# Kernel optimization log

Measured on AMD Instinct MI355X. Metric: run time of the kernel, lower is better.

Reference implementation:

```python
import jax, jax.numpy as jnp
import numpy as np

# ---- hash-grid encoder constants (instant-NGP style, nr_levels=24 from source) ----
L_LEVELS = 24
F_FEAT = 2
T_SIZE = 1 << 19          # hashmap entries per level
BASE_RES = 16
MAX_RES = 2048
IN_CH = 3
N_PTS = 524288
GEOM = 32
MIN_OFFSET = 1e-4
BB = 2.0                  # bb_sides
RES = np.floor(BASE_RES * np.exp(np.arange(L_LEVELS) * np.log(MAX_RES / BASE_RES) / (L_LEVELS - 1))).astype(np.float32)


def hash_encode(points, table):
    # points: [N,3] in bb [-BB/2, BB/2]; table: [L, T, F]
    N = points.shape[0]
    x = points / BB + 0.5                         # normalize to [0,1]
    res = jnp.asarray(RES)                        # [L]
    scaled = x[None, :, :] * res[:, None, None]   # [L,N,3]
    pos0f = jnp.floor(scaled)
    frac = scaled - pos0f                         # [L,N,3]
    pos0 = pos0f.astype(jnp.uint32)
    p0 = jnp.uint32(1); p1 = jnp.uint32(2654435761); p2 = jnp.uint32(805459861)
    mask = jnp.uint32(T_SIZE - 1)
    lvl = jnp.arange(L_LEVELS)[:, None]
    out = jnp.zeros((L_LEVELS, N, F_FEAT), points.dtype)
    for corner in range(8):                       # fixed 8-corner trilinear loop
        off = np.array([(corner >> d) & 1 for d in range(3)])
        c = pos0 + jnp.asarray(off, dtype=jnp.uint32)
        idx = ((c[..., 0] * p0) ^ (c[..., 1] * p1) ^ (c[..., 2] * p2)) & mask  # [L,N]
        feats = table[lvl, idx.astype(jnp.int32)]                              # [L,N,F]
        w = jnp.prod(jnp.where(jnp.asarray(off, bool), frac, 1.0 - frac), axis=-1)  # [L,N]
        out = out + w[..., None] * feats
    return out.transpose(1, 0, 2).reshape(N, L_LEVELS * F_FEAT)  # [N, 48]


def setup_inputs() -> dict:
    key = jax.random.key(0)
    ks = jax.random.split(key, 12)
    points = jax.random.uniform(ks[0], (N_PTS, IN_CH), dtype=jnp.float32)
    hash_table = jax.random.uniform(ks[1], (L_LEVELS, T_SIZE, F_FEAT), jnp.float32, -1e-4, 1e-4)
    D_ENC = L_LEVELS * F_FEAT  # 48
    def lin(k, fi, fo):
        kw, kb = jax.random.split(k)
        return (jax.random.normal(kw, (fi, fo), jnp.float32) / np.sqrt(fi),
                jax.random.normal(kb, (fo,), jnp.float32) * 0.01)
    W0, b0 = lin(ks[2], D_ENC, 32)
    W1, b1 = lin(ks[3], 32, 32)
    W2, b2 = lin(ks[4], 32, 32)
    W3, b3 = lin(ks[5], 32, 1 + GEOM)
    # two per-offset MLPs (geom_feat -> 32 -> 1), batched as grouped weights [K=2,...]
    eps_W0 = jax.random.normal(ks[6], (2, GEOM, 32), jnp.float32) / np.sqrt(GEOM)
    eps_b0 = jax.random.normal(ks[7], (2, 32), jnp.float32) * 0.01
    eps_W1 = jax.random.normal(ks[8], (2, 32, 1), jnp.float32) / np.sqrt(32)
    eps_b1 = jax.random.normal(ks[9], (2, 1), jnp.float32) * 0.01
    return {"points": points, "hash_table": hash_table,
            "W0": W0, "b0": b0, "W1": W1, "b1": b1, "W2": W2, "b2": b2, "W3": W3, "b3": b3,
            "eps_W0": eps_W0, "eps_b0": eps_b0, "eps_W1": eps_W1, "eps_b1": eps_b1}


def reference(points, hash_table, W0, b0, W1, b1, W2, b2, W3, b3, eps_W0, eps_b0, eps_W1, eps_b1):
    enc = hash_encode(points, hash_table)                 # [N,48]
    h = jax.nn.relu(enc @ W0 + b0)
    h = jax.nn.relu(h @ W1 + b1)
    h = jax.nn.relu(h @ W2 + b2)
    pred = h @ W3 + b3                                    # [N, 1+GEOM]
    sdf = pred[:, 0:1]                                    # [N,1]
    geom_feats = pred[:, 1:]                              # [N,GEOM]
    # grouped per-offset MLPs: k indexes the 2 offset heads
    he = jax.nn.relu(jnp.einsum('nf,kfh->nkh', geom_feats, eps_W0) + eps_b0[None])
    eps = (jnp.einsum('nkh,kho->nko', he, eps_W1) + eps_b1[None]).squeeze(-1)  # [N,2]
    nr_outer = 1
    inner_eps = jax.nn.softplus(eps[:, nr_outer:])        # [N,1]
    outer_eps = -jax.nn.softplus(eps[:, :nr_outer])       # [N,1]
    cum_outer = jnp.cumsum(outer_eps, axis=1) - MIN_OFFSET
    cum_inner = jnp.flip(jnp.cumsum(inner_eps, axis=1) + MIN_OFFSET, axis=1)
    sdfs = jnp.concatenate([sdf + cum_inner, sdf, sdf + cum_outer], axis=1)[..., None]   # [N,3,1]
    offsets = jnp.concatenate([inner_eps, jnp.zeros_like(sdf), outer_eps], axis=1)[..., None]
    return sdfs, offsets, geom_feats
```

## Files before the change

### kernel.cpp

```cpp
#include <hip/hip_runtime.h>
#include <math.h>
#include <stdint.h>

#define NPTS   524288
#define TSZ    524288u
#define HMASK  (TSZ - 1u)
#define PRIME1 2654435761u
#define PRIME2 805459861u
#define NLVL   24

typedef float    v4f __attribute__((ext_vector_type(4)));
typedef _Float16 v4h __attribute__((ext_vector_type(4)));

#define MFMA16(A,B,C) __builtin_amdgcn_mfma_f32_16x16x16f16((A),(B),(C),0,0,0)

struct ResParams { float r[NLVL]; };

__device__ __forceinline__ uint32_t pack_f16x2(float a, float b) {
    union { _Float16 h[2]; uint32_t u; } c;
    c.h[0] = (_Float16)a; c.h[1] = (_Float16)b;
    return c.u;
}

__device__ __forceinline__ float softplus_f(float x) {
    return fmaxf(x, 0.f) + log1pf(expf(-fabsf(x)));
}

__global__ __launch_bounds__(256)
void hash_gather_pass(const float* __restrict__ points,
                      const float* __restrict__ table,
                      uint32_t* __restrict__ enc, ResParams rp)
{
    const int bid   = blockIdx.x;
    const int xcd   = bid & 7;
    const int j     = bid >> 3;
    const int lvl   = ((j >> 9) << 3) + xcd;
    const int chunk = j & 511;
    const float res = rp.r[lvl];
    const float* __restrict__ tl = table + (size_t)lvl * (size_t)(TSZ * 2u);
    uint32_t* __restrict__ el = enc + (size_t)lvl * (size_t)NPTS;
    const int pbase = chunk * 1024 + threadIdx.x;

    #pragma unroll
    for (int k = 0; k < 4; ++k) {
        const int p = pbase + k * 256;
        const float x0 = points[p * 3 + 0] * 0.5f + 0.5f;
        const float y0 = points[p * 3 + 1] * 0.5f + 0.5f;
        const float z0 = points[p * 3 + 2] * 0.5f + 0.5f;
        const float sx = x0 * res, sy = y0 * res, sz = z0 * res;
        const float fx = floorf(sx), fy = floorf(sy), fz = floorf(sz);
        const float tx = sx - fx,  ty = sy - fy,  tz = sz - fz;
        const uint32_t cx = (uint32_t)fx, cy = (uint32_t)fy, cz = (uint32_t)fz;
        const uint32_t hy0 = cy * PRIME1, hy1 = (cy + 1u) * PRIME1;
        const uint32_t hz0 = cz * PRIME2, hz1 = (cz + 1u) * PRIME2;
        const float wy[2] = {1.f - ty, ty};
        const float wz[2] = {1.f - tz, tz};
        const float wx0 = 1.f - tx, wx1 = tx;
        const bool cx_even = (cx & 1u) == 0u;

        float a0 = 0.f, a1 = 0.f;
        #pragma unroll
        for (int yz = 0; yz < 4; ++yz) {
            const uint32_t dy = (uint32_t)(yz & 1);
            const uint32_t dz = (uint32_t)(yz >> 1);
            const uint32_t h  = (dy ? hy1 : hy0) ^ (dz ? hz1 : hz0);
            const uint32_t i0 = (cx ^ h) & HMASK;
            const uint32_t i1 = ((cx + 1u) ^ h) & HMASK;
            float e0x, e0y, e1x, e1y;
            if (cx_even) {
                const float4 f4 = *reinterpret_cast<const float4*>(tl + (size_t)(i0 & ~1u) * 2u);
                const bool lo = (i0 & 1u) == 0u;
                e0x = lo ? f4.x : f4.z;  e0y = lo ? f4.y : f4.w;
                e1x = lo ? f4.z : f4.x;  e1y = lo ? f4.w : f4.y;
            } else {
                const float2 fa = *reinterpret_cast<const float2*>(tl + (size_t)i0 * 2u);
                const float2 fb = *reinterpret_cast<const float2*>(tl + (size_t)i1 * 2u);
                e0x = fa.x; e0y = fa.y; e1x = fb.x; e1y = fb.y;
            }
            const float wyz = wy[dy] * wz[dz];
            const float w0 = wyz * wx0, w1 = wyz * wx1;
            a0 = fmaf(w0, e0x, fmaf(w1, e1x, a0));
            a1 = fmaf(w0, e0y, fmaf(w1, e1y, a1));
        }
        el[p] = pack_f16x2(a0 * 1024.f, a1 * 1024.f);
    }
}

#define SW0T   0
#define SW1T   3328
#define SW2T   5632
#define SW3T   7936
#define SET    11392
#define SB0    18048
#define SB1    18176
#define SB2    18304
#define SB3    18432
#define SEB0   18624
#define SEW1   18880
#define SEB1   19136
#define SGEOM  19152
#define SMB    28368

__global__ __launch_bounds__(256)
void mlp_mfma(const uint32_t* __restrict__ enc,
              const float* __restrict__ W0, const float* __restrict__ b0,
              const float* __restrict__ W1, const float* __restrict__ b1,
              const float* __restrict__ W2, const float* __restrict__ b2,
              const float* __restrict__ W3, const float* __restrict__ b3,
              const float* __restrict__ eW0, const float* __restrict__ eb0,
              const float* __restrict__ eW1, const float* __restrict__ eb1,
              float* __restrict__ out)
{
    __shared__ __align__(16) unsigned char sm[SMB];
    _Float16* const w0t = (_Float16*)(sm + SW0T);
    _Float16* const w1t = (_Float16*)(sm + SW1T);
    _Float16* const w2t = (_Float16*)(sm + SW2T);
    _Float16* const w3t = (_Float16*)(sm + SW3T);
    _Float16* const et  = (_Float16*)(sm + SET);
    float* const b0s  = (float*)(sm + SB0);
    float* const b1s  = (float*)(sm + SB1);
    float* const b2s  = (float*)(sm + SB2);
    float* const b3s  = (float*)(sm + SB3);
    float* const eb0s = (float*)(sm + SEB0);
    float* const ew1s = (float*)(sm + SEW1);
    float* const eb1s = (float*)(sm + SEB1);

    const int tid = threadIdx.x;

    for (int i = tid; i < 1536; i += 256) { const int k = i >> 5, o = i & 31;
        w0t[o * 52 + k] = (_Float16)(W0[i] * (1.f / 1024.f)); }
    for (int i = tid; i < 1024; i += 256) { const int k = i >> 5, o = i & 31;
        w1t[o * 36 + k] = (_Float16)W1[i];
        w2t[o * 36 + k] = (_Float16)W2[i]; }
    for (int i = tid; i < 1536; i += 256) { const int o = i >> 5, k = i & 31;
        w3t[o * 36 + k] = (o < 33) ? (_Float16)W3[k * 33 + o] : (_Float16)0.f; }
    for (int i = tid; i < 3328; i += 256) {
        const int hd = i / 1664, rem = i - hd * 1664;
        const int hh = rem / 52, o = rem % 52;
        et[i] = (o >= 1 && o <= 32) ? (_Float16)eW0[hd * 1024 + (o - 1) * 32 + hh]
                                    : (_Float16)0.f;
    }
    for (int i = tid; i < 32; i += 256) { b0s[i] = b0[i]; b1s[i] = b1[i]; b2s[i] = b2[i]; }
    for (int i = tid; i < 48; i += 256) { b3s[i] = (i < 33) ? b3[i] : 0.f; }
    for (int i = tid; i < 64; i += 256) { eb0s[i] = eb0[i]; ew1s[i] = eW1[i]; }
    if (tid < 2) eb1s[tid] = eb1[tid];
    __syncthreads();

    const int wv = tid >> 6, l = tid & 63, g = l >> 4, lm = l & 15;
    const size_t ptbase = (size_t)blockIdx.x * 256 + (size_t)wv * 64;

    v4h bx[4][3];
    #pragma unroll
    for (int tt = 0; tt < 4; ++tt) {
        const size_t pt = ptbase + tt * 16 + lm;
        #pragma unroll
        for (int kc = 0; kc < 3; ++kc) {
            const int lv = 8 * kc + 2 * g;
            union { uint32_t u[2]; v4h h; } c;
            c.u[0] = enc[(size_t)lv * NPTS + pt];
            c.u[1] = enc[(size_t)(lv + 1) * NPTS + pt];
            bx[tt][kc] = c.h;
        }
    }

    v4f acc[2][4];
    #pragma unroll
    for (int m = 0; m < 2; ++m) {
        const v4f bi = *(const v4f*)(b0s + 16 * m + 4 * g);
        const v4h a0f = *(const v4h*)(w0t + (16 * m + lm) * 52 + 4 * g);
        const v4h a1f = *(const v4h*)(w0t + (16 * m + lm) * 52 + 16 + 4 * g);
        const v4h a2f = *(const v4h*)(w0t + (16 * m + lm) * 52 + 32 + 4 * g);
        #pragma unroll
        for (int tt = 0; tt < 4; ++tt) {
            v4f a = bi;
            a = MFMA16(a0f, bx[tt][0], a);
            a = MFMA16(a1f, bx[tt][1], a);
            a = MFMA16(a2f, bx[tt][2], a);
            acc[m][tt] = a;
        }
    }
    v4h bh[4][2];
    #pragma unroll
    for (int tt = 0; tt < 4; ++tt)
        #pragma unroll
        for (int m = 0; m < 2; ++m) {
            v4h h;
            #pragma unroll
            for (int r = 0; r < 4; ++r) h[r] = (_Float16)fmaxf(acc[m][tt][r], 0.f);
            bh[tt][m] = h;
        }

    #pragma unroll
    for (int m = 0; m < 2; ++m) {
        const v4f bi = *(const v4f*)(b1s + 16 * m + 4 * g);
        const v4h a0f = *(const v4h*)(w1t + (16 * m + lm) * 36 + 4 * g);
        const v4h a1f = *(const v4h*)(w1t + (16 * m + lm) * 36 + 16 + 4 * g);
        #pragma unroll
        for (int tt = 0; tt < 4; ++tt) {
            v4f a = bi;
            a = MFMA16(a0f, bh[tt][0], a);
            a = MFMA16(a1f, bh[tt][1], a);
            acc[m][tt] = a;
        }
    }
    #pragma unroll
    for (int tt = 0; tt < 4; ++tt)
        #pragma unroll
        for (int m = 0; m < 2; ++m) {
            v4h h;
            #pragma unroll
            for (int r = 0; r < 4; ++r) h[r] = (_Float16)fmaxf(acc[m][tt][r], 0.f);
            bh[tt][m] = h;
        }

    #pragma unroll
    for (int m = 0; m < 2; ++m) {
        const v4f bi = *(const v4f*)(b2s + 16 * m + 4 * g);
        const v4h a0f = *(const v4h*)(w2t + (16 * m + lm) * 36 + 4 * g);
        const v4h a1f = *(const v4h*)(w2t + (16 * m + lm) * 36 + 16 + 4 * g);
        #pragma unroll
        for (int tt = 0; tt < 4; ++tt) {
            v4f a = bi;
            a = MFMA16(a0f, bh[tt][0], a);
            a = MFMA16(a1f, bh[tt][1], a);
            acc[m][tt] = a;
        }
    }
    #pragma unroll
    for (int tt = 0; tt < 4; ++tt)
        #pragma unroll
        for (int m = 0; m < 2; ++m) {
            v4h h;
            #pragma unroll
            for (int r = 0; r < 4; ++r) h[r] = (_Float16)fmaxf(acc[m][tt][r], 0.f);
            bh[tt][m] = h;
        }

    v4f acc3[3][4];
    #pragma unroll
    for (int m = 0; m < 3; ++m) {
        const v4f bi = *(const v4f*)(b3s + 16 * m + 4 * g);
        const v4h a0f = *(const v4h*)(w3t + (16 * m + lm) * 36 + 4 * g);
        const v4h a1f = *(const v4h*)(w3t + (16 * m + lm) * 36 + 16 + 4 * g);
        #pragma unroll
        for (int tt = 0; tt < 4; ++tt) {
            v4f a = bi;
            a = MFMA16(a0f, bh[tt][0], a);
            a = MFMA16(a1f, bh[tt][1], a);
            acc3[m][tt] = a;
        }
    }
    v4h pf[4][3];
    #pragma unroll
    for (int tt = 0; tt < 4; ++tt)
        #pragma unroll
        for (int m = 0; m < 3; ++m) {
            v4h h;
            #pragma unroll
            for (int r = 0; r < 4; ++r) h[r] = (_Float16)acc3[m][tt][r];
            pf[tt][m] = h;
        }

    float ep[2][4];
    #pragma unroll
    for (int k = 0; k < 2; ++k) {
        const v4f bi0 = *(const v4f*)(eb0s + k * 32 + 4 * g);
        const v4f bi1 = *(const v4f*)(eb0s + k * 32 + 16 + 4 * g);
        const v4f w10 = *(const v4f*)(ew1s + k * 32 + 4 * g);
        const v4f w11 = *(const v4f*)(ew1s + k * 32 + 16 + 4 * g);
        const _Float16* eb = et + (size_t)k * 1664;
        const v4h e00 = *(const v4h*)(eb + lm * 52 + 4 * g);
        const v4h e01 = *(const v4h*)(eb + lm * 52 + 16 + 4 * g);
        const v4h e02 = *(const v4h*)(eb + lm * 52 + 32 + 4 * g);
        const v4h e10 = *(const v4h*)(eb + (16 + lm) * 52 + 4 * g);
        const v4h e11 = *(const v4h*)(eb + (16 + lm) * 52 + 16 + 4 * g);
        const v4h e12 = *(const v4h*)(eb + (16 + lm) * 52 + 32 + 4 * g);
        #pragma unroll
        for (int tt = 0; tt < 4; ++tt) {
            v4f h0 = bi0, h1 = bi1;
            h0 = MFMA16(e00, pf[tt][0], h0);
            h0 = MFMA16(e01, pf[tt][1], h0);
            h0 = MFMA16(e02, pf[tt][2], h0);
            h1 = MFMA16(e10, pf[tt][0], h1);
            h1 = MFMA16(e11, pf[tt][1], h1);
            h1 = MFMA16(e12, pf[tt][2], h1);
            float p = fmaxf(h0[0], 0.f) * w10[0] + fmaxf(h0[1], 0.f) * w10[1]
                    + fmaxf(h0[2], 0.f) * w10[2] + fmaxf(h0[3], 0.f) * w10[3]
                    + fmaxf(h1[0], 0.f) * w11[0] + fmaxf(h1[1], 0.f) * w11[1]
                    + fmaxf(h1[2], 0.f) * w11[2] + fmaxf(h1[3], 0.f) * w11[3];
            p += __shfl_xor(p, 16);
            p += __shfl_xor(p, 32);
            ep[k][tt] = p + eb1s[k];
        }
    }

    float* const gw = (float*)(sm + SGEOM) + wv * (16 * 36);
    #pragma unroll
    for (int tt = 0; tt < 4; ++tt) {
        #pragma unroll
        for (int m = 0; m < 3; ++m)
            #pragma unroll
            for (int r = 0; r < 4; ++r) {
                const int o = 16 * m + 4 * g + r;
                if (o >= 1 && o <= 32) gw[lm * 36 + o - 1] = acc3[m][tt][r];
            }
        __syncthreads();
        {
            const int pl = l >> 2, q = l & 3;
            const v4f g0 = *(const v4f*)(gw + pl * 36 + q * 8);
            const v4f g1 = *(const v4f*)(gw + pl * 36 + q * 8 + 4);
            float* og = out + (size_t)NPTS * 6 + (ptbase + tt * 16 + pl) * 32 + q * 8;
            *reinterpret_cast<v4f*>(og)     = g0;
            *reinterpret_cast<v4f*>(og + 4) = g1;
        }
        if (l < 16) {
            const size_t pid = ptbase + tt * 16 + l;
            const float sdf   = acc3[0][tt][0];
            const float inner = softplus_f(ep[1][tt]);
            const float outer = -softplus_f(ep[0][tt]);
            out[pid * 3 + 0] = sdf + inner + 1e-4f;
            out[pid * 3 + 1] = sdf;
            out[pid * 3 + 2] = sdf + outer - 1e-4f;
            float* oo = out + (size_t)NPTS * 3 + pid * 3;
            oo[0] = inner; oo[1] = 0.f; oo[2] = outer;
        }
        __syncthreads();
    }
}

extern "C" void kernel_launch(void* const* d_in, const int* in_sizes, int n_in,
                              void* d_out, int out_size, void* d_ws, size_t ws_size,
                              hipStream_t stream) {
    const float* points = (const float*)d_in[0];
    const float* table  = (const float*)d_in[1];
    const float* W0  = (const float*)d_in[2];
    const float* b0  = (const float*)d_in[3];
    const float* W1  = (const float*)d_in[4];
    const float* b1  = (const float*)d_in[5];
    const float* W2  = (const float*)d_in[6];
    const float* b2  = (const float*)d_in[7];
    const float* W3  = (const float*)d_in[8];
    const float* b3  = (const float*)d_in[9];
    const float* eW0 = (const float*)d_in[10];
    const float* eb0 = (const float*)d_in[11];
    const float* eW1 = (const float*)d_in[12];
    const float* eb1 = (const float*)d_in[13];
    float* out = (float*)d_out;

    ResParams rp;
    for (int l = 0; l < NLVL; ++l)
        rp.r[l] = (float)floor(16.0 * exp((double)l * log(2048.0 / 16.0) / 23.0));
    (void)in_sizes; (void)n_in; (void)out_size; (void)ws_size;

    uint32_t* enc = (uint32_t*)d_ws;
    hash_gather_pass<<<dim3(NLVL * 512), dim3(256), 0, stream>>>(points, table, enc, rp);
    mlp_mfma<<<dim3(NPTS / 256), dim3(256), 0, stream>>>(
        enc, W0, b0, W1, b1, W2, b2, W3, b3, eW0, eb0, eW1, eb1, out);
}
```

Measured before the change: 316.0 us.

## Sort points by Morton bucket before hash gather for table locality

Adds a histogram, scan and scatter pipeline that reorders points into 32^3 Morton-ordered spatial buckets. The hash gather then runs on the sorted points, and the MLP writes results back through the permutation. The aim is better cache locality for the random hash-table lookups, since nearby points share grid corners on the coarse levels. In exchange it adds three small kernels, a memset, atomics and scattered output writes, and it only runs when the workspace is large enough.

Result: no change. 321.6 us (+1.8%).

```diff
diff --git a/kernel.cpp b/kernel.cpp
--- a/kernel.cpp
+++ b/kernel.cpp
@@ -8,6 +8,7 @@
 #define PRIME1 2654435761u
 #define PRIME2 805459861u
 #define NLVL   24
+#define NBKT   32768
 
 typedef float    v4f __attribute__((ext_vector_type(4)));
 typedef _Float16 v4h __attribute__((ext_vector_type(4)));
@@ -24,6 +25,66 @@
 
 __device__ __forceinline__ float softplus_f(float x) {
     return fmaxf(x, 0.f) + log1pf(expf(-fabsf(x)));
+}
+
+__device__ __forceinline__ uint32_t part1by2(uint32_t x) {
+    x &= 0x3FFu;
+    x = (x | (x << 16)) & 0x030000FFu;
+    x = (x | (x << 8))  & 0x0300F00Fu;
+    x = (x | (x << 4))  & 0x030C30C3u;
+    x = (x | (x << 2))  & 0x09249249u;
+    return x;
+}
+__device__ __forceinline__ uint32_t bucket_of(float px, float py, float pz) {
+    const uint32_t bx = min(31u, (uint32_t)(px * 32.f));
+    const uint32_t by = min(31u, (uint32_t)(py * 32.f));
+    const uint32_t bz = min(31u, (uint32_t)(pz * 32.f));
+    return part1by2(bx) | (part1by2(by) << 1) | (part1by2(bz) << 2);
+}
+
+__global__ __launch_bounds__(256)
+void hist_pass(const float* __restrict__ pts, uint32_t* __restrict__ hist) {
+    int p = blockIdx.x * 1024 + threadIdx.x;
+    #pragma unroll
+    for (int k = 0; k < 4; ++k, p += 256) {
+        const uint32_t b = bucket_of(pts[p * 3 + 0], pts[p * 3 + 1], pts[p * 3 + 2]);
+        atomicAdd(&hist[b], 1u);
+    }
+}
+
+__global__ __launch_bounds__(1024)
+void scan_pass(const uint32_t* __restrict__ hist, uint32_t* __restrict__ cursor) {
+    __shared__ uint32_t tsum[1024];
+    const int t = threadIdx.x;
+    uint32_t local[32];
+    uint32_t s = 0;
+    #pragma unroll
+    for (int i = 0; i < 32; ++i) { local[i] = s; s += hist[t * 32 + i]; }
+    tsum[t] = s;
+    __syncthreads();
+    for (int off = 1; off < 1024; off <<= 1) {
+        const uint32_t v = (t >= off) ? tsum[t - off] : 0u;
+        __syncthreads();
+        tsum[t] += v;
+        __syncthreads();
+    }
+    const uint32_t base = (t == 0) ? 0u : tsum[t - 1];
+    #pragma unroll
+    for (int i = 0; i < 32; ++i) cursor[t * 32 + i] = base + local[i];
+}
+
+__global__ __launch_bounds__(256)
+void scatter_pass(const float* __restrict__ pts, uint32_t* __restrict__ cursor,
+                  float* __restrict__ spts, uint32_t* __restrict__ perm) {
+    int p = blockIdx.x * 1024 + threadIdx.x;
+    #pragma unroll
+    for (int k = 0; k < 4; ++k, p += 256) {
+        const float px = pts[p * 3 + 0], py = pts[p * 3 + 1], pz = pts[p * 3 + 2];
+        const uint32_t b = bucket_of(px, py, pz);
+        const uint32_t d = atomicAdd(&cursor[b], 1u);
+        spts[d * 3 + 0] = px; spts[d * 3 + 1] = py; spts[d * 3 + 2] = pz;
+        perm[d] = (uint32_t)p;
+    }
 }
 
 __global__ __launch_bounds__(256)
@@ -103,6 +164,7 @@
 
 __global__ __launch_bounds__(256)
 void mlp_mfma(const uint32_t* __restrict__ enc,
+              const uint32_t* __restrict__ perm,
               const float* __restrict__ W0, const float* __restrict__ b0,
               const float* __restrict__ W1, const float* __restrict__ b1,
               const float* __restrict__ W2, const float* __restrict__ b2,
@@ -307,14 +369,17 @@
         __syncthreads();
         {
             const int pl = l >> 2, q = l & 3;
+            const size_t s = ptbase + tt * 16 + pl;
+            const size_t opid = perm ? (size_t)perm[s] : s;
             const v4f g0 = *(const v4f*)(gw + pl * 36 + q * 8);
             const v4f g1 = *(const v4f*)(gw + pl * 36 + q * 8 + 4);
-            float* og = out + (size_t)NPTS * 6 + (ptbase + tt * 16 + pl) * 32 + q * 8;
+            float* og = out + (size_t)NPTS * 6 + opid * 32 + q * 8;
             *reinterpret_cast<v4f*>(og)     = g0;
             *reinterpret_cast<v4f*>(og + 4) = g1;
         }
         if (l < 16) {
-            const size_t pid = ptbase + tt * 16 + l;
+            const size_t s = ptbase + tt * 16 + l;
+            const size_t pid = perm ? (size_t)perm[s] : s;
             const float sdf   = acc3[0][tt][0];
             const float inner = softplus_f(ep[1][tt]);
             const float outer = -softplus_f(ep[0][tt]);
@@ -350,10 +415,33 @@
     ResParams rp;
     for (int l = 0; l < NLVL; ++l)
         rp.r[l] = (float)floor(16.0 * exp((double)l * log(2048.0 / 16.0) / 23.0));
-    (void)in_sizes; (void)n_in; (void)out_size; (void)ws_size;
+    (void)in_sizes; (void)n_in; (void)out_size;
+
+    const size_t ENC_B  = (size_t)NLVL * NPTS * 4;
+    const size_t SPTS_B = (size_t)NPTS * 3 * 4;
+    const size_t PERM_B = (size_t)NPTS * 4;
+    const size_t HIST_B = (size_t)NBKT * 4;
+    const size_t WS_NEEDED = ENC_B + SPTS_B + PERM_B + 2 * HIST_B;
 
     uint32_t* enc = (uint32_t*)d_ws;
-    hash_gather_pass<<<dim3(NLVL * 512), dim3(256), 0, stream>>>(points, table, enc, rp);
-    mlp_mfma<<<dim3(NPTS / 256), dim3(256), 0, stream>>>(
-        enc, W0, b0, W1, b1, W2, b2, W3, b3, eW0, eb0, eW1, eb1, out);
-}
+
+    if (ws_size >= WS_NEEDED) {
+        float*    spts   = (float*)((char*)d_ws + ENC_B);
+        uint32_t* perm   = (uint32_t*)((char*)d_ws + ENC_B + SPTS_B);
+        uint32_t* hist   = (uint32_t*)((char*)d_ws + ENC_B + SPTS_B + PERM_B);
+        uint32_t* cursor = (uint32_t*)((char*)d_ws + ENC_B + SPTS_B + PERM_B + HIST_B);
+
+        hipMemsetAsync(hist, 0, HIST_B, stream);
+        hist_pass<<<dim3(NPTS / 1024), dim3(256), 0, stream>>>(points, hist);
+        scan_pass<<<dim3(1), dim3(1024), 0, stream>>>(hist, cursor);
+        scatter_pass<<<dim3(NPTS / 1024), dim3(256), 0, stream>>>(points, cursor, spts, perm);
+        hash_gather_pass<<<dim3(NLVL * 512), dim3(256), 0, stream>>>(spts, table, enc, rp);
+        mlp_mfma<<<dim3(NPTS / 256), dim3(256), 0, stream>>>(
+            enc, perm, W0, b0, W1, b1, W2, b2, W3, b3, eW0, eb0, eW1, eb1, out);
+    } else {
+        hash_gather_pass<<<dim3(NLVL * 512), dim3(256), 0, stream>>>(points, table, enc, rp);
+        mlp_mfma<<<dim3(NPTS / 256), dim3(256), 0, stream>>>(
+            enc, (const uint32_t*)nullptr, W0, b0, W1, b1, W2, b2, W3, b3,
+            eW0, eb0, eW1, eb1, out);
+    }
+}
```
